# Performance work log

Measured on AMD Instinct MI355X. Metric: run time of the kernel, lower is better.

The kernel has to match this reference:

```python
import jax, jax.numpy as jnp
import numpy as np


def setup_inputs() -> dict:
    key = jax.random.key(0)
    k1, k2, k3, k4, k5 = jax.random.split(key, 5)
    B, S, T = 256, 512, 64
    emissions = jax.random.normal(k1, (B, S, T), dtype=jnp.float32)
    tags = jax.random.randint(k2, (B, S), 0, T, dtype=jnp.int64)
    mask = jnp.ones((B, S), dtype=jnp.int32)
    init_range = 0.1
    start_transitions = jax.random.uniform(k3, (T,), minval=-init_range, maxval=init_range, dtype=jnp.float32)
    end_transitions = jax.random.uniform(k4, (T,), minval=-init_range, maxval=init_range, dtype=jnp.float32)
    transitions = jax.random.uniform(k5, (T, T), minval=-init_range, maxval=init_range, dtype=jnp.float32)
    return {"emissions": emissions, "tags": tags, "mask": mask,
            "start_transitions": start_transitions,
            "end_transitions": end_transitions,
            "transitions": transitions}


def _crf_nll_mean(emissions, tags, mask, start_transitions, end_transitions, transitions):
    # batch_first -> time-major: [S, B, T], [S, B]
    em = jnp.transpose(emissions, (1, 0, 2))
    tg = jnp.transpose(tags, (1, 0))
    mk = jnp.transpose(mask, (1, 0))
    maskf = mk.astype(em.dtype)                      # [S, B]
    S, B, T = em.shape
    batch_idx = jnp.arange(B)

    # ---- numerator: score of the gold path (fully vectorized) ----
    emit = jnp.take_along_axis(em, tg[:, :, None], axis=2)[..., 0]   # [S, B]
    trans_sc = transitions[tg[:-1], tg[1:]]                          # [S-1, B]
    score_num = start_transitions[tg[0]] + emit[0]
    score_num = score_num + jnp.sum((trans_sc + emit[1:]) * maskf[1:], axis=0)
    seq_ends = jnp.sum(mk, axis=0) - 1                               # [B]
    last_tags = tg[seq_ends, batch_idx]
    score_num = score_num + end_transitions[last_tags]

    # ---- denominator: log-partition via logsumexp scan ----
    init = start_transitions + em[0]                                 # [B, T]

    def step(score, xs):
        em_i, m_i = xs                                               # [B,T], [B]
        # [B, T_prev, T_next]
        next_score = score[:, :, None] + transitions[None, :, :] + em_i[:, None, :]
        next_score = jax.nn.logsumexp(next_score, axis=1)
        score = jnp.where(m_i[:, None] != 0, next_score, score)
        return score, None

    final, _ = jax.lax.scan(step, init, (em[1:], mk[1:]))
    denom = jax.nn.logsumexp(final + end_transitions, axis=1)        # [B]

    llh = denom - score_num                                          # [B]
    return jnp.mean(llh)                                             # reduction='mean'


def reference(emissions, tags, mask, start_transitions, end_transitions, transitions):
    return _crf_nll_mean(emissions, tags, mask, start_transitions, end_transitions, transitions)
```

## Files before the change

### kernel.cpp

```cpp
#include <hip/hip_runtime.h>

#define BATCH 256
#define SEQ   512
#define NT    64
#define PCH   8
#define CLEN  64
#define PITCH 68
#define SLICE_CH 16384

typedef __attribute__((ext_vector_type(8)))  short bf16x8;
typedef __attribute__((ext_vector_type(16))) float f32x16;
typedef __attribute__((ext_vector_type(4)))  float f32x4;
typedef __attribute__((ext_vector_type(2)))  float f32x2;

static __device__ __forceinline__ unsigned pk_bf16(float lo, float hi) {
    return __builtin_amdgcn_perm(__float_as_uint(hi), __float_as_uint(lo), 0x07060302u);
}
static __device__ __forceinline__ short bf16_trunc(float v) {
    return (short)(__float_as_uint(v) >> 16);
}

__global__ __launch_bounds__(1024, 4) void crf_fused(
    const float* __restrict__ emissions,
    const int*   __restrict__ tags,
    const int*   __restrict__ mask,
    const float* __restrict__ start_tr,
    const float* __restrict__ end_tr,
    const float* __restrict__ trans,
    float* __restrict__ ws_head,
    float* __restrict__ out)
{
    __shared__ __align__(16) unsigned char smem[PCH * SLICE_CH];
    __shared__ __align__(16) float r_lds[NT];
    __shared__ float score_lds;

    const int tid  = threadIdx.x;
    const int lane = tid & 63;
    const int wv   = tid >> 6;
    const int b    = blockIdx.x;
    const int c    = wv >> 1;
    const int nt   = wv & 1;

    unsigned char* slice = smem + c * SLICE_CH;
    float*          w_flat = (float*)slice;
    unsigned short* ldsT   = (unsigned short*)slice;

    const int h  = lane >> 5;
    const int ml = lane & 31;

    const int s0 = c * CLEN;
    int L = (SEQ - 1) - s0; if (L > CLEN) L = CLEN;

    const float* em_b = emissions + (size_t)b * SEQ * NT;

    {
        const float4* src = (const float4*)(em_b + (size_t)(s0 + 1) * NT);
        float4*       dst = (float4*)w_flat;
        const int total4 = L * (NT / 4);
        for (int i = nt * 64 + lane; i < total4; i += 128) {
            float4 v = src[i];
            v.x = __expf(v.x); v.y = __expf(v.y);
            v.z = __expf(v.z); v.w = __expf(v.w);
            dst[i] = v;
        }
    }

    bf16x8 Af[2][4];
#pragma unroll
    for (int mt = 0; mt < 2; ++mt) {
        int m = mt * 32 + ml;
#pragma unroll
        for (int kk = 0; kk < 4; ++kk) {
            bf16x8 f;
#pragma unroll
            for (int j = 0; j < 8; ++j) {
                int r = 32 * (kk >> 1) + 16 * (kk & 1) + (j & 3) + 8 * (j >> 2) + 4 * h;
                f[j] = bf16_trunc(__expf(trans[r * NT + m]) * 0.0078125f);
            }
            Af[mt][kk] = f;
        }
    }

    union BU { unsigned u[4]; bf16x8 v; };
    BU Bv[4];
    {
        int n = nt * 32 + ml;
#pragma unroll
        for (int kk = 0; kk < 4; ++kk)
#pragma unroll
            for (int d = 0; d < 4; ++d) {
                int j0 = 2 * d;
                int r0 = 32 * (kk >> 1) + 16 * (kk & 1) + (j0 & 3) + 8 * (j0 >> 2) + 4 * h;
                unsigned lo = (r0     == n) ? 0x3f80u : 0u;
                unsigned hi = (r0 + 1 == n) ? 0x3f80u : 0u;
                Bv[kk].u[d] = lo | (hi << 16);
            }
    }

    __syncthreads();

    const f32x16 zf = {};

    for (int s = 0; s < L; ++s) {
        const float* wrow = w_flat + s * NT;
        f32x4 wq[4][2];
#pragma unroll
        for (int kk = 0; kk < 4; ++kk) {
            int base = 32 * (kk >> 1) + 16 * (kk & 1) + 4 * h;
            wq[kk][0] = *(const f32x4*)(wrow + base);
            wq[kk][1] = *(const f32x4*)(wrow + base + 8);
        }

        __builtin_amdgcn_s_setprio(1);
        f32x16 a0 = __builtin_amdgcn_mfma_f32_32x32x16_bf16(Af[0][0], Bv[0].v, zf, 0, 0, 0);
        f32x16 a1 = __builtin_amdgcn_mfma_f32_32x32x16_bf16(Af[1][0], Bv[0].v, zf, 0, 0, 0);
#pragma unroll
        for (int kk = 1; kk < 4; ++kk) {
            a0 = __builtin_amdgcn_mfma_f32_32x32x16_bf16(Af[0][kk], Bv[kk].v, a0, 0, 0, 0);
            a1 = __builtin_amdgcn_mfma_f32_32x32x16_bf16(Af[1][kk], Bv[kk].v, a1, 0, 0, 0);
        }
        __builtin_amdgcn_s_setprio(0);

#pragma unroll
        for (int kk = 0; kk < 4; ++kk) {
            const int qo = 8 * (kk & 1);
            const f32x4 wa = wq[kk][0], wb = wq[kk][1];
#pragma unroll
            for (int d = 0; d < 4; ++d) {
                const int j0 = 2 * d;
                float w0 = (d < 2) ? wa[j0]     : wb[j0 - 4];
                float w1 = (d < 2) ? wa[j0 + 1] : wb[j0 - 3];
                f32x2 av, wvv;
                if (kk < 2) { av[0] = a0[qo + j0]; av[1] = a0[qo + j0 + 1]; }
                else        { av[0] = a1[qo + j0]; av[1] = a1[qo + j0 + 1]; }
                wvv[0] = w0; wvv[1] = w1;
                f32x2 p = av * wvv;
                Bv[kk].u[d] = pk_bf16(p[0], p[1]);
            }
        }
    }

    __syncthreads();
    {
        int n = nt * 32 + ml;
#pragma unroll
        for (int kk = 0; kk < 4; ++kk)
#pragma unroll
            for (int d = 0; d < 4; ++d) {
                int j0 = 2 * d;
                int r0 = 32 * (kk >> 1) + 16 * (kk & 1) + (j0 & 3) + 8 * (j0 >> 2) + 4 * h;
                *(unsigned*)&ldsT[n * PITCH + r0] = Bv[kk].u[d];
            }
    }
    __syncthreads();

    const int j = lane;
    float denom = 0.f;

    if (wv == 1) {
        const int* tg_b = tags + b * SEQ;
        const int* mk_b = mask + b * SEQ;
        float part = 0.f;
        int mcount = 0;
        for (int s = j; s < SEQ; s += 64) {
            int m = mk_b[s];
            mcount += m;
            int t = tg_b[s];
            if (s == 0) {
                part += start_tr[t] + em_b[t];
            } else {
                int tp = tg_b[s - 1];
                float v = trans[tp * NT + t] + em_b[s * NT + t];
                part += m ? v : 0.f;
            }
        }
#pragma unroll
        for (int d = 32; d; d >>= 1) {
            part   += __shfl_xor(part, d);
            mcount += __shfl_xor(mcount, d);
        }
        if (j == 0) score_lds = part + end_tr[tg_b[mcount - 1]];
    } else if (wv == 0) {
        float r = __expf(end_tr[j]);
        r_lds[j] = r;
        __threadfence_block();
        int X = 0;

        for (int cc = PCH - 1; cc >= 0; --cc) {
            const unsigned short* Trow = (const unsigned short*)(smem + cc * SLICE_CH) + j * PITCH;
            float a0 = 0.f, a1 = 0.f, a2 = 0.f, a3 = 0.f;
#pragma unroll
            for (int u = 0; u < 8; ++u) {
                uint2 q0 = *(const uint2*)(Trow + u * 8);
                uint2 q1 = *(const uint2*)(Trow + u * 8 + 4);
                f32x4 ra = *(const f32x4*)&r_lds[u * 8];
                f32x4 rb = *(const f32x4*)&r_lds[u * 8 + 4];
                a0 = fmaf(ra[0], __uint_as_float(q0.x << 16),         a0);
                a1 = fmaf(ra[1], __uint_as_float(q0.x & 0xffff0000u), a1);
                a2 = fmaf(ra[2], __uint_as_float(q0.y << 16),         a2);
                a3 = fmaf(ra[3], __uint_as_float(q0.y & 0xffff0000u), a3);
                a0 = fmaf(rb[0], __uint_as_float(q1.x << 16),         a0);
                a1 = fmaf(rb[1], __uint_as_float(q1.x & 0xffff0000u), a1);
                a2 = fmaf(rb[2], __uint_as_float(q1.y << 16),         a2);
                a3 = fmaf(rb[3], __uint_as_float(q1.y & 0xffff0000u), a3);
            }
            float rn = (a0 + a1) + (a2 + a3);
            unsigned eb = (__builtin_amdgcn_readfirstlane((int)__float_as_uint(rn)) >> 23) & 0xffu;
            r = rn * __uint_as_float((254u - eb) << 23);
            X += (int)eb - 127;
            r_lds[j] = r;
            __threadfence_block();
        }

        float u0 = __expf(start_tr[j] + em_b[j]);
        float v = r * u0;
#pragma unroll
        for (int d = 32; d; d >>= 1) v += __shfl_xor(v, d);
        denom = __logf(v) + (float)(X + 7 * (SEQ - 1)) * 0.6931471805599453f;
    }

    __syncthreads();

    if (wv == 0 && j == 0) {
        float llh = denom - score_lds;
        atomicAdd(&ws_head[0], llh * (1.0f / BATCH));
        __threadfence();
        unsigned old = atomicAdd((unsigned*)ws_head + 1, 1u);
        if (old == BATCH - 1) {
            __threadfence();
            out[0] = atomicAdd(&ws_head[0], 0.0f);
        }
    }
}

extern "C" void kernel_launch(void* const* d_in, const int* in_sizes, int n_in,
                              void* d_out, int out_size, void* d_ws, size_t ws_size,
                              hipStream_t stream) {
    const float* emissions = (const float*)d_in[0];
    const int*   tags      = (const int*)d_in[1];
    const int*   mask      = (const int*)d_in[2];
    const float* start_tr  = (const float*)d_in[3];
    const float* end_tr    = (const float*)d_in[4];
    const float* trans     = (const float*)d_in[5];

    float* ws_head = (float*)d_ws;

    hipMemsetAsync(d_ws, 0, 256, stream);

    crf_fused<<<dim3(BATCH), 1024, 0, stream>>>(emissions, tags, mask,
                                                start_tr, end_tr, trans,
                                                ws_head, (float*)d_out);
}
```

Baseline: 146.0 us.

## Use one wave per sequence chunk covering both column halves, halving block size

Each chunk of the sequence was handled by two waves that each owned 32 of the 64 state columns. Now a single wave per chunk processes both column halves in sequence, so the block shrinks from 1024 to 512 threads. The block-wide barriers around the chunk scan become wave-local fences, since each wave now touches only its own shared-memory slice. This removes cross-wave barrier cost and lets the two independent MFMA chains interleave within one wave. In exchange each wave does twice the serial MFMA and packing work per step and holds more registers.

```diff
diff --git a/kernel.cpp b/kernel.cpp
--- a/kernel.cpp
+++ b/kernel.cpp
@@ -20,7 +20,7 @@
     return (short)(__float_as_uint(v) >> 16);
 }
 
-__global__ __launch_bounds__(1024, 4) void crf_fused(
+__global__ __launch_bounds__(512, 2) void crf_fused(
     const float* __restrict__ emissions,
     const int*   __restrict__ tags,
     const int*   __restrict__ mask,
@@ -38,12 +38,11 @@
     const int lane = tid & 63;
     const int wv   = tid >> 6;
     const int b    = blockIdx.x;
-    const int c    = wv >> 1;
-    const int nt   = wv & 1;
+    const int c    = wv;
 
     unsigned char* slice = smem + c * SLICE_CH;
-    float*          w_flat = (float*)slice;
-    unsigned short* ldsT   = (unsigned short*)slice;
+    float (*w_lds)[NT]   = (float (*)[NT])slice;
+    unsigned short* ldsT = (unsigned short*)slice;
 
     const int h  = lane >> 5;
     const int ml = lane & 31;
@@ -55,9 +54,9 @@
 
     {
         const float4* src = (const float4*)(em_b + (size_t)(s0 + 1) * NT);
-        float4*       dst = (float4*)w_flat;
+        float4*       dst = (float4*)slice;
         const int total4 = L * (NT / 4);
-        for (int i = nt * 64 + lane; i < total4; i += 128) {
+        for (int i = lane; i < total4; i += 64) {
             float4 v = src[i];
             v.x = __expf(v.x); v.y = __expf(v.y);
             v.z = __expf(v.z); v.w = __expf(v.w);
@@ -82,27 +81,28 @@
     }
 
     union BU { unsigned u[4]; bf16x8 v; };
-    BU Bv[4];
-    {
-        int n = nt * 32 + ml;
-#pragma unroll
-        for (int kk = 0; kk < 4; ++kk)
+    BU Bv[4][2];
+#pragma unroll
+    for (int kk = 0; kk < 4; ++kk)
+#pragma unroll
+        for (int nt = 0; nt < 2; ++nt) {
+            int n = nt * 32 + ml;
 #pragma unroll
             for (int d = 0; d < 4; ++d) {
                 int j0 = 2 * d;
                 int r0 = 32 * (kk >> 1) + 16 * (kk & 1) + (j0 & 3) + 8 * (j0 >> 2) + 4 * h;
                 unsigned lo = (r0     == n) ? 0x3f80u : 0u;
                 unsigned hi = (r0 + 1 == n) ? 0x3f80u : 0u;
-                Bv[kk].u[d] = lo | (hi << 16);
-            }
-    }
-
-    __syncthreads();
+                Bv[kk][nt].u[d] = lo | (hi << 16);
+            }
+        }
+
+    __threadfence_block();
 
     const f32x16 zf = {};
 
     for (int s = 0; s < L; ++s) {
-        const float* wrow = w_flat + s * NT;
+        const float* wrow = w_lds[s];
         f32x4 wq[4][2];
 #pragma unroll
         for (int kk = 0; kk < 4; ++kk) {
@@ -111,47 +111,52 @@
             wq[kk][1] = *(const f32x4*)(wrow + base + 8);
         }
 
-        __builtin_amdgcn_s_setprio(1);
-        f32x16 a0 = __builtin_amdgcn_mfma_f32_32x32x16_bf16(Af[0][0], Bv[0].v, zf, 0, 0, 0);
-        f32x16 a1 = __builtin_amdgcn_mfma_f32_32x32x16_bf16(Af[1][0], Bv[0].v, zf, 0, 0, 0);
-#pragma unroll
-        for (int kk = 1; kk < 4; ++kk) {
-            a0 = __builtin_amdgcn_mfma_f32_32x32x16_bf16(Af[0][kk], Bv[kk].v, a0, 0, 0, 0);
-            a1 = __builtin_amdgcn_mfma_f32_32x32x16_bf16(Af[1][kk], Bv[kk].v, a1, 0, 0, 0);
-        }
-        __builtin_amdgcn_s_setprio(0);
-
-#pragma unroll
-        for (int kk = 0; kk < 4; ++kk) {
-            const int qo = 8 * (kk & 1);
-            const f32x4 wa = wq[kk][0], wb = wq[kk][1];
-#pragma unroll
-            for (int d = 0; d < 4; ++d) {
-                const int j0 = 2 * d;
-                float w0 = (d < 2) ? wa[j0]     : wb[j0 - 4];
-                float w1 = (d < 2) ? wa[j0 + 1] : wb[j0 - 3];
-                f32x2 av, wvv;
-                if (kk < 2) { av[0] = a0[qo + j0]; av[1] = a0[qo + j0 + 1]; }
-                else        { av[0] = a1[qo + j0]; av[1] = a1[qo + j0 + 1]; }
-                wvv[0] = w0; wvv[1] = w1;
-                f32x2 p = av * wvv;
-                Bv[kk].u[d] = pk_bf16(p[0], p[1]);
-            }
-        }
-    }
-
-    __syncthreads();
-    {
-        int n = nt * 32 + ml;
-#pragma unroll
-        for (int kk = 0; kk < 4; ++kk)
+#pragma unroll
+        for (int nt = 0; nt < 2; ++nt) {
+            __builtin_amdgcn_s_setprio(1);
+            f32x16 a0 = __builtin_amdgcn_mfma_f32_32x32x16_bf16(Af[0][0], Bv[0][nt].v, zf, 0, 0, 0);
+            f32x16 a1 = __builtin_amdgcn_mfma_f32_32x32x16_bf16(Af[1][0], Bv[0][nt].v, zf, 0, 0, 0);
+#pragma unroll
+            for (int kk = 1; kk < 4; ++kk) {
+                a0 = __builtin_amdgcn_mfma_f32_32x32x16_bf16(Af[0][kk], Bv[kk][nt].v, a0, 0, 0, 0);
+                a1 = __builtin_amdgcn_mfma_f32_32x32x16_bf16(Af[1][kk], Bv[kk][nt].v, a1, 0, 0, 0);
+            }
+            __builtin_amdgcn_s_setprio(0);
+
+#pragma unroll
+            for (int kk = 0; kk < 4; ++kk) {
+                const int qo = 8 * (kk & 1);
+                const f32x4 wa = wq[kk][0], wb = wq[kk][1];
+#pragma unroll
+                for (int d = 0; d < 4; ++d) {
+                    const int j0 = 2 * d;
+                    float w0 = (d < 2) ? wa[j0]     : wb[j0 - 4];
+                    float w1 = (d < 2) ? wa[j0 + 1] : wb[j0 - 3];
+                    f32x2 av, wvv;
+                    if (kk < 2) { av[0] = a0[qo + j0]; av[1] = a0[qo + j0 + 1]; }
+                    else        { av[0] = a1[qo + j0]; av[1] = a1[qo + j0 + 1]; }
+                    wvv[0] = w0; wvv[1] = w1;
+                    f32x2 p = av * wvv;
+                    Bv[kk][nt].u[d] = pk_bf16(p[0], p[1]);
+                }
+            }
+        }
+    }
+
+    __threadfence_block();
+#pragma unroll
+    for (int kk = 0; kk < 4; ++kk)
+#pragma unroll
+        for (int nt = 0; nt < 2; ++nt) {
+            int n = nt * 32 + ml;
 #pragma unroll
             for (int d = 0; d < 4; ++d) {
                 int j0 = 2 * d;
                 int r0 = 32 * (kk >> 1) + 16 * (kk & 1) + (j0 & 3) + 8 * (j0 >> 2) + 4 * h;
-                *(unsigned*)&ldsT[n * PITCH + r0] = Bv[kk].u[d];
-            }
-    }
+                *(unsigned*)&ldsT[n * PITCH + r0] = Bv[kk][nt].u[d];
+            }
+        }
+
     __syncthreads();
 
     const int j = lane;
@@ -247,7 +252,7 @@
 
     hipMemsetAsync(d_ws, 0, 256, stream);
 
-    crf_fused<<<dim3(BATCH), 1024, 0, stream>>>(emissions, tags, mask,
-                                                start_tr, end_tr, trans,
-                                                ws_head, (float*)d_out);
-}
+    crf_fused<<<dim3(BATCH), 512, 0, stream>>>(emissions, tags, mask,
+                                               start_tr, end_tr, trans,
+                                               ws_head, (float*)d_out);
+}
```

Result: faster. 141.7 us (-3.0%).
